# Optimization experiments

Measured on AMD Instinct MI355X. Metric: run time of the kernel, lower is better.

## Reference

```python
import jax, jax.numpy as jnp
import numpy as np

V = 100000          # vocab size
D = 256             # hidden dim
B, N = 32, 128      # batch, max_len
K = 100             # noise_ratio
NORM_TERM = 11.512925  # log(V), norm_term='auto'
BACKOFF_PROB = 1e-10


def setup_inputs() -> dict:
    key = jax.random.key(0)
    ks = jax.random.split(key, 6)
    target = jax.random.randint(ks[0], (B, N), 0, V)
    noise_samples = jax.random.randint(ks[1], (B, N, K), 0, V)
    hidden = jax.random.normal(ks[2], (B, N, D), dtype=jnp.float32) * 0.1
    weight = jax.random.normal(ks[3], (V, D), dtype=jnp.float32) * 0.05
    bias = jax.random.normal(ks[4], (V,), dtype=jnp.float32) * 0.01
    u = jax.random.uniform(ks[5], (V,), dtype=jnp.float32) + BACKOFF_PROB
    noise_probs = u / jnp.sum(u)  # normalized noise distribution
    return {"target": target, "noise_samples": noise_samples, "hidden": hidden,
            "weight": weight, "bias": bias, "noise_probs": noise_probs}


def reference(target, noise_samples, hidden, weight, bias, noise_probs):
    # score_noise = log P_noise(noise_samples)   (B,N,K) -- irregular gather on (V,)
    score_noise = jnp.log(noise_probs)[noise_samples]
    # get_score (IndexLinear): gathered output-embedding dot products
    w_t = weight[target]                                   # (B,N,D)
    score_model = jnp.einsum('bnd,bnd->bn', hidden, w_t) + bias[target] - NORM_TERM
    w_n = weight[noise_samples]                            # (B,N,K,D) big gather
    score_noise_in_model = (jnp.einsum('bnd,bnkd->bnk', hidden, w_n)
                            + bias[noise_samples] - NORM_TERM)
    # NCE binary classification loss (score_target_in_noise passed as zeros)
    log_k = jnp.log(jnp.float32(K))
    logit_true = score_model - log_k                        # (B,N) label=1
    logit_noise = score_noise_in_model - score_noise - log_k  # (B,N,K) label=0
    # BCE-with-logits: -log sigmoid(x) = softplus(-x); -log(1-sigmoid(x)) = softplus(x)
    loss = jax.nn.softplus(-logit_true) + jnp.sum(jax.nn.softplus(logit_noise), axis=-1)
    # reduction='elementwise_mean'
    return jnp.mean(loss)
```

## Files before the change

kernel.cpp:

```cpp
#include <hip/hip_runtime.h>
#include <math.h>

#define V 100000
#define D 256
#define B 32
#define N 128
#define K 100
#define NPOS (B * N)
#define NPAIR (NPOS * (K + 1))
#define BIN_ROWS 32
#define NBIN (V / BIN_ROWS)
#define NSHARD 16
#define CAP_S 32
#define MAXTOT (NSHARD * CAP_S)
#define BPB 3
#define NBLK ((NBIN + BPB - 1) / BPB)
#define ROW_W32 136
#define HVEC (NPOS * D / 4)
#define NORM_TERM 11.512925f
#define LOG_K 4.605170186f

typedef float    f32x4 __attribute__((ext_vector_type(4)));
typedef unsigned u32x2 __attribute__((ext_vector_type(2)));
typedef unsigned u32x4 __attribute__((ext_vector_type(4)));
typedef __fp16   f16x2 __attribute__((ext_vector_type(2)));

__device__ __forceinline__ float softplus(float x) {
    return fmaxf(x, 0.f) + __logf(1.f + __expf(-fabsf(x)));
}

__device__ __forceinline__ unsigned pack_f16(float a, float b) {
#if __has_builtin(__builtin_amdgcn_cvt_pkrtz)
    f16x2 h = __builtin_amdgcn_cvt_pkrtz(a, b);
#else
    f16x2 h; h.x = (__fp16)a; h.y = (__fp16)b;
#endif
    union { f16x2 h; unsigned u; } c; c.h = h;
    return c.u;
}

#if __has_builtin(__builtin_amdgcn_fdot2)
#define DOT2(a, b, c) __builtin_amdgcn_fdot2((a), (b), (c), false)
#else
__device__ __forceinline__ float DOT2(f16x2 a, f16x2 b, float c) {
    return fmaf((float)a.x, (float)b.x, fmaf((float)a.y, (float)b.y, c));
}
#endif

union V4H { u32x4 u; f16x2 h[4]; };

template <int CTRL>
__device__ __forceinline__ float dpp_add(float x) {
    int y = __builtin_amdgcn_update_dpp(__float_as_int(x), __float_as_int(x),
                                        CTRL, 0xF, 0xF, false);
    return x + __int_as_float(y);
}
__device__ __forceinline__ float quarter_sum(float x) {
    x = dpp_add<0xB1>(x);
    x = dpp_add<0x4E>(x);
    x = dpp_add<0x141>(x);
    x = dpp_add<0x140>(x);
    return x;
}

__global__ __launch_bounds__(256) void scatter_hconv_kernel(
    const int* __restrict__ target, const int* __restrict__ noise,
    const float* __restrict__ hidden,
    int* __restrict__ cursor, unsigned* __restrict__ buf,
    unsigned* __restrict__ htab32)
{
    const int p = blockIdx.x * 256 + threadIdx.x;

    int row, pos; unsigned flag;
    if (p < NPOS * K) { pos = p / K; row = noise[p]; flag = 0u; }
    else              { pos = p - NPOS * K; row = target[pos]; flag = 1u; }
    const int cell = (row >> 5) * NSHARD + (blockIdx.x & (NSHARD - 1));
    const int slot = atomicAdd(&cursor[cell], 1);
    if (slot < CAP_S)
        buf[(size_t)cell * CAP_S + slot] =
            ((unsigned)(row & (BIN_ROWS - 1)) << 13) | ((unsigned)pos << 1) | flag;

    if (p < HVEC) {
        const f32x4 h4 = *((const f32x4*)hidden + p);
        u32x2 o;
        o.x = pack_f16(h4.x, h4.y);
        o.y = pack_f16(h4.z, h4.w);
        *(u32x2*)(htab32 + (size_t)p * 2) = o;
    }
}

__global__ __launch_bounds__(256, 6) void compute_kernel(
    const unsigned* __restrict__ htab32, const float* __restrict__ weight,
    const float* __restrict__ bias, const float* __restrict__ noise_probs,
    const int* __restrict__ cursor, const unsigned* __restrict__ buf,
    float* __restrict__ out)
{
    __shared__ unsigned slab32[BIN_ROWS * ROW_W32];
    __shared__ float    sbias[BPB * BIN_ROWS];
    __shared__ float    slogp[BPB * BIN_ROWS];
    __shared__ unsigned plist[MAXTOT];
    __shared__ int      scnt[BPB * NSHARD];
    __shared__ int      pref[BPB][NSHARD + 1];
    __shared__ float    wsum[4];

    const int b0  = blockIdx.x * BPB;
    const int tid = threadIdx.x;
    const int wave = tid >> 6;
    const int lane = tid & 63;
    const int q    = lane >> 4;
    const int ql   = lane & 15;

    if (tid < BPB * NSHARD) {
        const int j = tid >> 4, s = tid & 15, bin = b0 + j;
        scnt[tid] = (bin < NBIN) ? min(cursor[bin * NSHARD + s], CAP_S) : 0;
    }
    __syncthreads();
    if (tid < BPB) {
        int s = 0;
        #pragma unroll
        for (int i = 0; i < NSHARD; ++i) { pref[tid][i] = s; s += scnt[tid * NSHARD + i]; }
        pref[tid][NSHARD] = s;
    }
    __syncthreads();

    for (int r = wave; r < BIN_ROWS; r += 4) {
        const f32x4 w4 = __builtin_nontemporal_load(
            (const f32x4*)(weight + (size_t)(b0 * BIN_ROWS + r) * D + lane * 4));
        u32x2 o;
        o.x = pack_f16(w4.x, w4.y);
        o.y = pack_f16(w4.z, w4.w);
        *(u32x2*)(slab32 + r * ROW_W32 + lane * 2) = o;
    }
    if (tid < BPB * BIN_ROWS) {
        const int j = tid >> 5, r = tid & 31, bin = b0 + j;
        if (bin < NBIN) {
            sbias[tid] = bias[bin * BIN_ROWS + r];
            slogp[tid] = __logf(noise_probs[bin * BIN_ROWS + r]);
        }
    }
    {
        const int total0 = pref[0][NSHARD];
        for (int i = tid; i < total0; i += 256) {
            int s = 0;
            #pragma unroll
            for (int m = 1; m < NSHARD; ++m) s += (i >= pref[0][m]);
            plist[i] = buf[((size_t)(b0 * NSHARD + s)) * CAP_S + (i - pref[0][s])];
        }
    }
    __syncthreads();

    float loss = 0.f;
    for (int j = 0; j < BPB; ++j) {
        const int bin   = b0 + j;
        const int total = (bin < NBIN) ? pref[j][NSHARD] : 0;
        const bool hasnext = (j + 1 < BPB) && (bin + 1 < NBIN);

        f32x4 wpre[8];
        if (hasnext) {
            const float* wsrc = weight + (size_t)(bin + 1) * BIN_ROWS * D;
            #pragma unroll
            for (int i = 0; i < 8; ++i)
                wpre[i] = __builtin_nontemporal_load(
                    (const f32x4*)(wsrc + (size_t)(wave + 4 * i) * D + lane * 4));
        }
        unsigned pl_a = 0u, pl_b = 0u; int tot_n = 0;
        if (hasnext) {
            tot_n = pref[j + 1][NSHARD];
            if (tid < tot_n) {
                int s = 0;
                #pragma unroll
                for (int m = 1; m < NSHARD; ++m) s += (tid >= pref[j + 1][m]);
                pl_a = buf[((size_t)((bin + 1) * NSHARD + s)) * CAP_S + (tid - pref[j + 1][s])];
            }
            if (tid + 256 < tot_n) {
                int s = 0;
                #pragma unroll
                for (int m = 1; m < NSHARD; ++m) s += (tid + 256 >= pref[j + 1][m]);
                pl_b = buf[((size_t)((bin + 1) * NSHARD + s)) * CAP_S + (tid + 256 - pref[j + 1][s])];
            }
        }

        for (int base = wave * 4; base < total; base += 16) {
            const int p = base + q;
            const bool valid = (p < total);
            const unsigned rec = valid ? plist[p] : 0u;
            const int rloc = (int)((rec >> 13) & (BIN_ROWS - 1));
            const int pos  = (int)((rec >> 1) & (NPOS - 1));

            const u32x4* hp = (const u32x4*)(htab32 + (size_t)pos * 128) + ql;
            V4H H0, H1, W0, W1;
            H0.u = hp[0];
            H1.u = hp[16];
            const unsigned* wr = slab32 + rloc * ROW_W32;
            W0.u = *(const u32x4*)(wr + ql * 4);
            W1.u = *(const u32x4*)(wr + 64 + ql * 4);

            float a0 = 0.f, a1 = 0.f, a2 = 0.f, a3 = 0.f;
            a0 = DOT2(H0.h[0], W0.h[0], a0);
            a1 = DOT2(H0.h[1], W0.h[1], a1);
            a2 = DOT2(H0.h[2], W0.h[2], a2);
            a3 = DOT2(H0.h[3], W0.h[3], a3);
            a0 = DOT2(H1.h[0], W1.h[0], a0);
            a1 = DOT2(H1.h[1], W1.h[1], a1);
            a2 = DOT2(H1.h[2], W1.h[2], a2);
            a3 = DOT2(H1.h[3], W1.h[3], a3);

            const float r = quarter_sum((a0 + a1) + (a2 + a3));

            const float score = r + sbias[j * BIN_ROWS + rloc] - NORM_TERM;
            const float x = (rec & 1u) ? (LOG_K - score)
                                       : (score - slogp[j * BIN_ROWS + rloc] - LOG_K);
            if (valid && ql == 0) loss += softplus(x);
        }
        __syncthreads();

        if (hasnext) {
            #pragma unroll
            for (int i = 0; i < 8; ++i) {
                u32x2 o;
                o.x = pack_f16(wpre[i].x, wpre[i].y);
                o.y = pack_f16(wpre[i].z, wpre[i].w);
                *(u32x2*)(slab32 + (wave + 4 * i) * ROW_W32 + lane * 2) = o;
            }
            if (tid < tot_n)       plist[tid]       = pl_a;
            if (tid + 256 < tot_n) plist[tid + 256] = pl_b;
        }
        __syncthreads();
    }

    loss += __shfl_xor(loss, 16, 64);
    loss += __shfl_xor(loss, 32, 64);
    if (lane == 0) wsum[wave] = loss;
    __syncthreads();
    if (tid == 0)
        atomicAdd(out, (wsum[0] + wsum[1] + wsum[2] + wsum[3])
                       * (1.0f / (float)NPOS));
}

extern "C" void kernel_launch(void* const* d_in, const int* in_sizes, int n_in,
                              void* d_out, int out_size, void* d_ws, size_t ws_size,
                              hipStream_t stream) {
    const int*   target      = (const int*)d_in[0];
    const int*   noise       = (const int*)d_in[1];
    const float* hidden      = (const float*)d_in[2];
    const float* weight      = (const float*)d_in[3];
    const float* bias        = (const float*)d_in[4];
    const float* noise_probs = (const float*)d_in[5];
    float* out = (float*)d_out;

    const size_t cursor_bytes = (size_t)NBIN * NSHARD * 4;
    const size_t buf_bytes    = (size_t)NBIN * NSHARD * CAP_S * 4;
    int*      cursor = (int*)d_ws;
    unsigned* buf    = (unsigned*)((char*)d_ws + cursor_bytes);
    unsigned* htab32 = (unsigned*)((char*)d_ws + cursor_bytes + buf_bytes);

    (void)hipMemsetAsync(cursor, 0, cursor_bytes, stream);
    (void)hipMemsetAsync(out, 0, sizeof(float), stream);

    scatter_hconv_kernel<<<NPAIR / 256, 256, 0, stream>>>(
        target, noise, hidden, cursor, buf, htab32);
    compute_kernel<<<NBLK, 256, 0, stream>>>(
        htab32, weight, bias, noise_probs, cursor, buf, out);
}
```

Before: 207.6 us.

## Replace sharded atomic bucketing with histogram, prefix-scan, and counting-sort placement

Replaces the single atomic scatter into fixed-capacity sharded bins with a multi-kernel counting sort. Per-block shared-memory histograms are scanned across blocks and bins, and a place kernel then writes records into a contiguous buffer. The compute kernel reads contiguous per-bin ranges and drops the shard prefix computation and the per-shard capacity truncation. In exchange it adds three extra kernel launches and a large per-block count matrix (404×3125 words), including a serial single-block scan.

```diff
diff --git a/kernel.cpp b/kernel.cpp
--- a/kernel.cpp
+++ b/kernel.cpp
@@ -10,9 +10,9 @@
 #define NPAIR (NPOS * (K + 1))
 #define BIN_ROWS 32
 #define NBIN (V / BIN_ROWS)
-#define NSHARD 16
-#define CAP_S 32
-#define MAXTOT (NSHARD * CAP_S)
+#define NSBLK 404
+#define PPB 1024
+#define MAXTOT 512
 #define BPB 3
 #define NBLK ((NBIN + BPB - 1) / BPB)
 #define ROW_W32 136
@@ -63,44 +63,127 @@
     return x;
 }
 
-__global__ __launch_bounds__(256) void scatter_hconv_kernel(
+__device__ __forceinline__ void decode_pair(
+    int p, const int* __restrict__ target, const int* __restrict__ noise,
+    int& row, int& pos, unsigned& flag)
+{
+    if (p < NPOS * K) { pos = p / K; row = noise[p]; flag = 0u; }
+    else              { pos = p - NPOS * K; row = target[pos]; flag = 1u; }
+}
+
+__global__ __launch_bounds__(256) void hist_hconv_kernel(
     const int* __restrict__ target, const int* __restrict__ noise,
     const float* __restrict__ hidden,
-    int* __restrict__ cursor, unsigned* __restrict__ buf,
+    unsigned* __restrict__ cnt ,
     unsigned* __restrict__ htab32)
 {
-    const int p = blockIdx.x * 256 + threadIdx.x;
-
-    int row, pos; unsigned flag;
-    if (p < NPOS * K) { pos = p / K; row = noise[p]; flag = 0u; }
-    else              { pos = p - NPOS * K; row = target[pos]; flag = 1u; }
-    const int cell = (row >> 5) * NSHARD + (blockIdx.x & (NSHARD - 1));
-    const int slot = atomicAdd(&cursor[cell], 1);
-    if (slot < CAP_S)
-        buf[(size_t)cell * CAP_S + slot] =
-            ((unsigned)(row & (BIN_ROWS - 1)) << 13) | ((unsigned)pos << 1) | flag;
-
-    if (p < HVEC) {
-        const f32x4 h4 = *((const f32x4*)hidden + p);
+    __shared__ unsigned hist[NBIN];
+    const int blk = blockIdx.x, tid = threadIdx.x;
+    for (int i = tid; i < NBIN; i += 256) hist[i] = 0u;
+    __syncthreads();
+    #pragma unroll
+    for (int i = 0; i < 4; ++i) {
+        const int p = blk * PPB + i * 256 + tid;
+        int row, pos; unsigned flag;
+        decode_pair(p, target, noise, row, pos, flag);
+        atomicAdd(&hist[row >> 5], 1u);
+    }
+    __syncthreads();
+    for (int i = tid; i < NBIN; i += 256)
+        cnt[(size_t)blk * NBIN + i] = hist[i];
+
+    for (int i = blk * 256 + tid; i < HVEC; i += NSBLK * 256) {
+        const f32x4 h4 = *((const f32x4*)hidden + i);
         u32x2 o;
         o.x = pack_f16(h4.x, h4.y);
         o.y = pack_f16(h4.z, h4.w);
-        *(u32x2*)(htab32 + (size_t)p * 2) = o;
+        *(u32x2*)(htab32 + (size_t)i * 2) = o;
+    }
+}
+
+__global__ __launch_bounds__(256) void scan_blocks_kernel(
+    unsigned* __restrict__ cnt, unsigned* __restrict__ total)
+{
+    const int wave = threadIdx.x >> 6, lane = threadIdx.x & 63;
+    const int bin = blockIdx.x * 4 + wave;
+    if (bin >= NBIN) return;
+    unsigned carry = 0u;
+    #pragma unroll
+    for (int i = 0; i < (NSBLK + 63) / 64; ++i) {
+        const int blk = i * 64 + lane;
+        unsigned x = (blk < NSBLK) ? cnt[(size_t)blk * NBIN + bin] : 0u;
+        unsigned incl = x;
+        #pragma unroll
+        for (int off = 1; off < 64; off <<= 1) {
+            unsigned y = __shfl_up(incl, off, 64);
+            if (lane >= off) incl += y;
+        }
+        if (blk < NSBLK) cnt[(size_t)blk * NBIN + bin] = incl - x + carry;
+        carry += __shfl(incl, 63, 64);
+    }
+    if (lane == 0) total[bin] = carry;
+}
+
+__global__ __launch_bounds__(256) void scan_bins_kernel(
+    const unsigned* __restrict__ total, unsigned* __restrict__ binbase)
+{
+    __shared__ unsigned wsums[4];
+    __shared__ unsigned carry_s;
+    const int tid = threadIdx.x, wave = tid >> 6, lane = tid & 63;
+    if (tid == 0) carry_s = 0u;
+    __syncthreads();
+    for (int it = 0; it < (NBIN + 256) / 256 + 1; ++it) {
+        const int idx = it * 256 + tid;
+        unsigned x = (idx < NBIN) ? total[idx] : 0u;
+        unsigned incl = x;
+        #pragma unroll
+        for (int off = 1; off < 64; off <<= 1) {
+            unsigned y = __shfl_up(incl, off, 64);
+            if (lane >= off) incl += y;
+        }
+        if (lane == 63) wsums[wave] = incl;
+        __syncthreads();
+        unsigned woff = carry_s;
+        for (int w = 0; w < wave; ++w) woff += wsums[w];
+        if (idx <= NBIN) binbase[idx] = incl - x + woff;
+        __syncthreads();
+        if (tid == 0) carry_s += wsums[0] + wsums[1] + wsums[2] + wsums[3];
+        __syncthreads();
+    }
+}
+
+__global__ __launch_bounds__(256) void place_kernel(
+    const int* __restrict__ target, const int* __restrict__ noise,
+    const unsigned* __restrict__ cnt, const unsigned* __restrict__ binbase,
+    unsigned* __restrict__ buf)
+{
+    __shared__ unsigned run[NBIN];
+    const int blk = blockIdx.x, tid = threadIdx.x;
+    for (int i = tid; i < NBIN; i += 256)
+        run[i] = binbase[i] + cnt[(size_t)blk * NBIN + i];
+    __syncthreads();
+    #pragma unroll
+    for (int i = 0; i < 4; ++i) {
+        const int p = blk * PPB + i * 256 + tid;
+        int row, pos; unsigned flag;
+        decode_pair(p, target, noise, row, pos, flag);
+        const unsigned slot = atomicAdd(&run[row >> 5], 1u);
+        buf[slot] = ((unsigned)(row & (BIN_ROWS - 1)) << 13)
+                  | ((unsigned)pos << 1) | flag;
     }
 }
 
 __global__ __launch_bounds__(256, 6) void compute_kernel(
     const unsigned* __restrict__ htab32, const float* __restrict__ weight,
     const float* __restrict__ bias, const float* __restrict__ noise_probs,
-    const int* __restrict__ cursor, const unsigned* __restrict__ buf,
+    const unsigned* __restrict__ binbase, const unsigned* __restrict__ buf,
     float* __restrict__ out)
 {
     __shared__ unsigned slab32[BIN_ROWS * ROW_W32];
     __shared__ float    sbias[BPB * BIN_ROWS];
     __shared__ float    slogp[BPB * BIN_ROWS];
     __shared__ unsigned plist[MAXTOT];
-    __shared__ int      scnt[BPB * NSHARD];
-    __shared__ int      pref[BPB][NSHARD + 1];
+    __shared__ unsigned sbase[BPB + 1];
     __shared__ float    wsum[4];
 
     const int b0  = blockIdx.x * BPB;
@@ -110,17 +193,7 @@
     const int q    = lane >> 4;
     const int ql   = lane & 15;
 
-    if (tid < BPB * NSHARD) {
-        const int j = tid >> 4, s = tid & 15, bin = b0 + j;
-        scnt[tid] = (bin < NBIN) ? min(cursor[bin * NSHARD + s], CAP_S) : 0;
-    }
-    __syncthreads();
-    if (tid < BPB) {
-        int s = 0;
-        #pragma unroll
-        for (int i = 0; i < NSHARD; ++i) { pref[tid][i] = s; s += scnt[tid * NSHARD + i]; }
-        pref[tid][NSHARD] = s;
-    }
+    if (tid <= BPB) sbase[tid] = binbase[min(b0 + tid, NBIN)];
     __syncthreads();
 
     for (int r = wave; r < BIN_ROWS; r += 4) {
@@ -139,20 +212,17 @@
         }
     }
     {
-        const int total0 = pref[0][NSHARD];
-        for (int i = tid; i < total0; i += 256) {
-            int s = 0;
-            #pragma unroll
-            for (int m = 1; m < NSHARD; ++m) s += (i >= pref[0][m]);
-            plist[i] = buf[((size_t)(b0 * NSHARD + s)) * CAP_S + (i - pref[0][s])];
-        }
+        const int start0 = sbase[0];
+        const int total0 = min((int)(sbase[1] - sbase[0]), MAXTOT);
+        for (int i = tid; i < total0; i += 256)
+            plist[i] = buf[start0 + i];
     }
     __syncthreads();
 
     float loss = 0.f;
     for (int j = 0; j < BPB; ++j) {
         const int bin   = b0 + j;
-        const int total = (bin < NBIN) ? pref[j][NSHARD] : 0;
+        const int total = min((int)(sbase[j + 1] - sbase[j]), MAXTOT);
         const bool hasnext = (j + 1 < BPB) && (bin + 1 < NBIN);
 
         f32x4 wpre[8];
@@ -165,19 +235,10 @@
         }
         unsigned pl_a = 0u, pl_b = 0u; int tot_n = 0;
         if (hasnext) {
-            tot_n = pref[j + 1][NSHARD];
-            if (tid < tot_n) {
-                int s = 0;
-                #pragma unroll
-                for (int m = 1; m < NSHARD; ++m) s += (tid >= pref[j + 1][m]);
-                pl_a = buf[((size_t)((bin + 1) * NSHARD + s)) * CAP_S + (tid - pref[j + 1][s])];
-            }
-            if (tid + 256 < tot_n) {
-                int s = 0;
-                #pragma unroll
-                for (int m = 1; m < NSHARD; ++m) s += (tid + 256 >= pref[j + 1][m]);
-                pl_b = buf[((size_t)((bin + 1) * NSHARD + s)) * CAP_S + (tid + 256 - pref[j + 1][s])];
-            }
+            const int start_n = sbase[j + 1];
+            tot_n = min((int)(sbase[j + 2] - sbase[j + 1]), MAXTOT);
+            if (tid < tot_n)       pl_a = buf[start_n + tid];
+            if (tid + 256 < tot_n) pl_b = buf[start_n + tid + 256];
         }
 
         for (int base = wave * 4; base < total; base += 16) {
@@ -248,17 +309,20 @@
     const float* noise_probs = (const float*)d_in[5];
     float* out = (float*)d_out;
 
-    const size_t cursor_bytes = (size_t)NBIN * NSHARD * 4;
-    const size_t buf_bytes    = (size_t)NBIN * NSHARD * CAP_S * 4;
-    int*      cursor = (int*)d_ws;
-    unsigned* buf    = (unsigned*)((char*)d_ws + cursor_bytes);
-    unsigned* htab32 = (unsigned*)((char*)d_ws + cursor_bytes + buf_bytes);
-
-    (void)hipMemsetAsync(cursor, 0, cursor_bytes, stream);
+    char* ws = (char*)d_ws;
+    unsigned* cnt     = (unsigned*)ws;                         ws += ((size_t)NSBLK * NBIN * 4 + 255) & ~255ull;
+    unsigned* total   = (unsigned*)ws;                         ws += ((size_t)NBIN * 4 + 255) & ~255ull;
+    unsigned* binbase = (unsigned*)ws;                         ws += ((size_t)(NBIN + 1) * 4 + 255) & ~255ull;
+    unsigned* buf     = (unsigned*)ws;                         ws += ((size_t)NPAIR * 4 + 255) & ~255ull;
+    unsigned* htab32  = (unsigned*)ws;
+
     (void)hipMemsetAsync(out, 0, sizeof(float), stream);
 
-    scatter_hconv_kernel<<<NPAIR / 256, 256, 0, stream>>>(
-        target, noise, hidden, cursor, buf, htab32);
+    hist_hconv_kernel<<<NSBLK, 256, 0, stream>>>(
+        target, noise, hidden, cnt, htab32);
+    scan_blocks_kernel<<<(NBIN + 3) / 4, 256, 0, stream>>>(cnt, total);
+    scan_bins_kernel<<<1, 256, 0, stream>>>(total, binbase);
+    place_kernel<<<NSBLK, 256, 0, stream>>>(target, noise, cnt, binbase, buf);
     compute_kernel<<<NBLK, 256, 0, stream>>>(
-        htab32, weight, bias, noise_probs, cursor, buf, out);
-}
+        htab32, weight, bias, noise_probs, binbase, buf, out);
+}
```

New measurement: 227.4 us. +9.6%, slower.
